# Performance work log

Hardware: AMD Instinct MI355X
Metric: run time of the kernel (lower is better)

The kernel has to match this reference:

```python
import jax, jax.numpy as jnp
import numpy as np

INPUT_SIZE = 24
OUTPUT_SIZE = 24
HIDDEN = 40
BATCH = 4096
SEQ = 256


def setup_inputs() -> dict:
    key = jax.random.key(0)
    ks = jax.random.split(key, 7)
    s = 1.0 / np.sqrt(HIDDEN)  # torch RNN/Linear default uniform bound
    x = jax.random.normal(ks[0], (BATCH, SEQ, INPUT_SIZE), dtype=jnp.float32)
    W_ih = jax.random.uniform(ks[1], (3 * HIDDEN, INPUT_SIZE), jnp.float32, -s, s)
    W_hh = jax.random.uniform(ks[2], (3 * HIDDEN, HIDDEN), jnp.float32, -s, s)
    b_ih = jax.random.uniform(ks[3], (3 * HIDDEN,), jnp.float32, -s, s)
    b_hh = jax.random.uniform(ks[4], (3 * HIDDEN,), jnp.float32, -s, s)
    W_fc = jax.random.uniform(ks[5], (OUTPUT_SIZE, HIDDEN), jnp.float32, -s, s)
    b_fc = jax.random.uniform(ks[6], (OUTPUT_SIZE,), jnp.float32, -s, s)
    return {"x": x, "W_ih": W_ih, "W_hh": W_hh, "b_ih": b_ih,
            "b_hh": b_hh, "W_fc": W_fc, "b_fc": b_fc}


def _gru_forward(x, W_ih, W_hh, b_ih, b_hh):
    # PyTorch GRU gate order: reset, update, new. Precompute input projections.
    B, T, _ = x.shape
    H = W_hh.shape[1]
    xg = jnp.einsum('bti,gi->btg', x, W_ih) + b_ih  # [B, T, 3H]

    def step(h, xg_t):
        hg = h @ W_hh.T + b_hh                      # [B, 3H]
        xr, xz, xn = jnp.split(xg_t, 3, axis=-1)
        hr, hz, hn = jnp.split(hg, 3, axis=-1)
        r = jax.nn.sigmoid(xr + hr)
        z = jax.nn.sigmoid(xz + hz)
        n = jnp.tanh(xn + r * hn)
        h_new = (1.0 - z) * n + z * h
        return h_new, h_new

    h0 = jnp.zeros((B, H), dtype=x.dtype)
    hT, outs = jax.lax.scan(step, h0, jnp.swapaxes(xg, 0, 1))  # outs: [T, B, H]
    return jnp.swapaxes(outs, 0, 1), hT                        # [B, T, H], [B, H]


def reference(x, W_ih, W_hh, b_ih, b_hh, W_fc, b_fc):
    seq_out, hT = _gru_forward(x, W_ih, W_hh, b_ih, b_hh)
    H = W_hh.shape[1]
    out = seq_out.reshape(-1, H)                   # [B*T, H]
    out = jax.nn.sigmoid(out @ W_fc.T + b_fc)      # [B*T, output_size]
    hidden = hT[None]                              # [n_layers=1, B, H]
    return out, hidden
```

## Files before the change

### kernel.cpp

```cpp
#include <hip/hip_runtime.h>
#include <math.h>

typedef __attribute__((ext_vector_type(8))) short short8;
typedef __attribute__((ext_vector_type(4))) float f32x4;

namespace {
constexpr int BATCH = 4096;
constexpr int SEQT  = 256;
constexpr int INSZ  = 24;
constexpr int H     = 40;
constexpr int NOUT  = 24;
constexpr int R     = 8;
constexpr int NT    = 256;

__device__ __forceinline__ unsigned short f2bf(float f) {
  unsigned int u = __float_as_uint(f);
  return (unsigned short)((u + 0x7FFFu + ((u >> 16) & 1u)) >> 16);
}
__device__ __forceinline__ unsigned short cvt_bf16(float f) {
  float r;
  asm("v_cvt_pk_bf16_f32 %0, %1, %2" : "=v"(r) : "v"(f), "v"(f));
  return (unsigned short)__float_as_uint(r);
}
__device__ __forceinline__ float4 ld4(const float* p) {
  return *reinterpret_cast<const float4*>(p);
}
__device__ __forceinline__ float sigm(float v) {
  return __builtin_amdgcn_rcpf(1.0f + __builtin_amdgcn_exp2f(v * -1.442695041f));
}
__device__ __forceinline__ float tanh_fast(float v) {
  return fmaf(2.0f,
              __builtin_amdgcn_rcpf(1.0f + __builtin_amdgcn_exp2f(v * -2.885390082f)),
              -1.0f);
}
}

#define BAR()                                              \
  asm volatile("s_waitcnt lgkmcnt(0)" ::: "memory");       \
  __builtin_amdgcn_s_barrier();                            \
  __builtin_amdgcn_sched_barrier(0);

__global__ __launch_bounds__(NT) void gru_mfma4(
    const float* __restrict__ x, const float* __restrict__ Wih,
    const float* __restrict__ Whh, const float* __restrict__ bih,
    const float* __restrict__ bhh, const float* __restrict__ Wfc,
    const float* __restrict__ bfc, float* __restrict__ out,
    float* __restrict__ hid) {
  __shared__ __align__(16) unsigned short Abuf[2 * 1024];

  const int tid = threadIdx.x;
  const int l   = tid & 63;
  const int w   = tid >> 6;
  const int lm  = l & 15;
  const int lq  = l >> 4;
  const int gb0 = blockIdx.x * R;

  reinterpret_cast<uint4*>(Abuf)[tid] = make_uint4(0, 0, 0, 0);

  const int aBase0 = ((lm * 64 + lq * 8)      ^ ((lm & 7) << 3));
  const int aBase1 = ((lm * 64 + lq * 8 + 32) ^ ((lm & 7) << 3));

  short8 B[4][2];
  float bias[4] = {0, 0, 0, 0};
  float hold[2] = {0, 0};
  int aw[2] = {0, 0};
  int u = 0;
  bool gvalid = false;
  if (w < 3) {
    u = w * 16 + lm;
    gvalid = (u < H);
#pragma unroll
    for (int z = 0; z < 4; ++z) {
#pragma unroll
      for (int kt = 0; kt < 2; ++kt) {
        short8 b;
#pragma unroll
        for (int j = 0; j < 8; ++j) {
          const int k = kt * 32 + lq * 8 + j;
          float v = 0.0f;
          if (gvalid) {
            if (z == 0)      v = (k < 24) ? Wih[u * 24 + k]          : Whh[u * 40 + (k - 24)];
            else if (z == 1) v = (k < 24) ? Wih[(40 + u) * 24 + k]   : Whh[(40 + u) * 40 + (k - 24)];
            else if (z == 2) v = (k < 24) ? Wih[(80 + u) * 24 + k]   : 0.0f;
            else             v = (k < 24) ? 0.0f                     : Whh[(80 + u) * 40 + (k - 24)];
          }
          b[j] = (short)f2bf(v);
        }
        B[z][kt] = b;
      }
    }
    if (gvalid) {
      bias[0] = bih[u] + bhh[u];
      bias[1] = bih[40 + u] + bhh[40 + u];
      bias[2] = bih[80 + u];
      bias[3] = bhh[80 + u];
    }
#pragma unroll
    for (int i = 0; i < 2; ++i) {
      const int arow = lq * 4 + i;
      aw[i] = ((arow * 64 + 24 + u) ^ ((arow & 7) << 3));
    }
  }

  short8 F[2][2];
  float biasF[2] = {0, 0};
  float* orow[2] = {nullptr, nullptr};
  const float* xp0 = nullptr;
  int xw0 = 0;
  bool xv = false;
  float4 xA0 = make_float4(0, 0, 0, 0), xB0 = make_float4(0, 0, 0, 0);
  if (w == 3) {
#pragma unroll
    for (int f = 0; f < 2; ++f) {
      const int o = f * 16 + lm;
#pragma unroll
      for (int kt = 0; kt < 2; ++kt) {
        short8 b;
#pragma unroll
        for (int j = 0; j < 8; ++j) {
          const int k = kt * 32 + lq * 8 + j;
          const float v = (o < NOUT && k >= 24) ? Wfc[o * H + (k - 24)] : 0.0f;
          b[j] = (short)f2bf(v);
        }
        F[f][kt] = b;
      }
      biasF[f] = (o < NOUT) ? bfc[o] : 0.0f;
    }
#pragma unroll
    for (int i = 0; i < 2; ++i)
      orow[i] = out + ((size_t)(gb0 + lq * 2 + i) * SEQT) * NOUT;

    xv = (l < 48);
    const int xr = l / 6, xc = (l - xr * 6) * 4;
    const int ar_ = ((xr >> 1) << 2) + (xr & 1);
    if (xv) xp0 = x + ((size_t)(gb0 + xr) * SEQT) * INSZ + xc;
    xw0 = ((ar_ * 64 + xc) ^ ((ar_ & 7) << 3));
  }

  __syncthreads();

  if (w == 3 && xv) {
    const float4 v0 = ld4(xp0);
    *reinterpret_cast<uint2*>(&Abuf[xw0]) = make_uint2(
        (unsigned)f2bf(v0.x) | ((unsigned)f2bf(v0.y) << 16),
        (unsigned)f2bf(v0.z) | ((unsigned)f2bf(v0.w) << 16));
    xA0 = ld4(xp0 + 1 * INSZ);
    xB0 = ld4(xp0 + 2 * INSZ);
  }
  __syncthreads();

#define GATE_STEP(BO, NBO)                                                      \
  if (w < 3) {                                                                  \
    const short8 A0 = *reinterpret_cast<const short8*>(&Abuf[(BO) + aBase0]);   \
    const short8 A1 = *reinterpret_cast<const short8*>(&Abuf[(BO) + aBase1]);   \
    f32x4 ar = {bias[0], bias[0], bias[0], bias[0]};                            \
    f32x4 az = {bias[1], bias[1], bias[1], bias[1]};                            \
    f32x4 ax = {bias[2], bias[2], bias[2], bias[2]};                            \
    f32x4 ah = {bias[3], bias[3], bias[3], bias[3]};                            \
    ar = __builtin_amdgcn_mfma_f32_16x16x32_bf16(A0, B[0][0], ar, 0, 0, 0);     \
    az = __builtin_amdgcn_mfma_f32_16x16x32_bf16(A0, B[1][0], az, 0, 0, 0);     \
    ax = __builtin_amdgcn_mfma_f32_16x16x32_bf16(A0, B[2][0], ax, 0, 0, 0);     \
    ah = __builtin_amdgcn_mfma_f32_16x16x32_bf16(A0, B[3][0], ah, 0, 0, 0);     \
    ar = __builtin_amdgcn_mfma_f32_16x16x32_bf16(A1, B[0][1], ar, 0, 0, 0);     \
    az = __builtin_amdgcn_mfma_f32_16x16x32_bf16(A1, B[1][1], az, 0, 0, 0);     \
    ah = __builtin_amdgcn_mfma_f32_16x16x32_bf16(A1, B[3][1], ah, 0, 0, 0);     \
    _Pragma("unroll")                                                           \
    for (int i = 0; i < 2; ++i) {                                               \
      const float rr = sigm(ar[i]);                                             \
      const float zz = sigm(az[i]);                                             \
      const float nn = tanh_fast(fmaf(rr, ah[i], ax[i]));                       \
      const float h  = fmaf(zz, hold[i] - nn, nn);                              \
      hold[i] = h;                                                              \
      if (gvalid) Abuf[(NBO) + aw[i]] = cvt_bf16(h);                            \
    }                                                                           \
  }

#define XSTAGE(T, TBO, XS)                                                      \
  if (xv) {                                                                     \
    if ((T) < SEQT) {                                                           \
      *reinterpret_cast<uint2*>(&Abuf[(TBO) + xw0]) = make_uint2(               \
          (unsigned)f2bf(XS.x) | ((unsigned)f2bf(XS.y) << 16),                  \
          (unsigned)f2bf(XS.z) | ((unsigned)f2bf(XS.w) << 16));                 \
    }                                                                           \
    if ((T) + 2 < SEQT) XS = ld4(xp0 + (size_t)((T) + 2) * INSZ);               \
  }

#define FC_STEP(T, BO)                                                          \
  {                                                                             \
    const short8 hA0 = *reinterpret_cast<const short8*>(&Abuf[(BO) + aBase0]);  \
    const short8 hA1 = *reinterpret_cast<const short8*>(&Abuf[(BO) + aBase1]);  \
    f32x4 f0 = {biasF[0], biasF[0], biasF[0], biasF[0]};                        \
    f32x4 f1 = {biasF[1], biasF[1], biasF[1], biasF[1]};                        \
    f0 = __builtin_amdgcn_mfma_f32_16x16x32_bf16(hA0, F[0][0], f0, 0, 0, 0);    \
    f1 = __builtin_amdgcn_mfma_f32_16x16x32_bf16(hA0, F[1][0], f1, 0, 0, 0);    \
    f0 = __builtin_amdgcn_mfma_f32_16x16x32_bf16(hA1, F[0][1], f0, 0, 0, 0);    \
    f1 = __builtin_amdgcn_mfma_f32_16x16x32_bf16(hA1, F[1][1], f1, 0, 0, 0);    \
    _Pragma("unroll")                                                           \
    for (int i = 0; i < 2; ++i) {                                               \
      orow[i][(size_t)(T) * NOUT + lm] = sigm(f0[i]);                           \
      if (lm < 8) orow[i][(size_t)(T) * NOUT + 16 + lm] = sigm(f1[i]);          \
    }                                                                           \
  }

  for (int tt = 0; tt < SEQT; tt += 2) {
    GATE_STEP(0, 1024)
    if (w == 3) {
      XSTAGE(tt + 1, 1024, xA0)
      if (tt > 0) FC_STEP(tt - 1, 0)
    }
    BAR()
    GATE_STEP(1024, 0)
    if (w == 3) {
      XSTAGE(tt + 2, 0, xB0)
      FC_STEP(tt, 1024)
    }
    BAR()
  }
  if (w == 3) FC_STEP(SEQT - 1, 0)

  if (w < 3 && gvalid) {
#pragma unroll
    for (int i = 0; i < 2; ++i)
      hid[(size_t)(gb0 + lq * 2 + i) * H + u] = hold[i];
  }
}

extern "C" void kernel_launch(void* const* d_in, const int* in_sizes, int n_in,
                              void* d_out, int out_size, void* d_ws, size_t ws_size,
                              hipStream_t stream) {
  const float* x   = (const float*)d_in[0];
  const float* Wih = (const float*)d_in[1];
  const float* Whh = (const float*)d_in[2];
  const float* bih = (const float*)d_in[3];
  const float* bhh = (const float*)d_in[4];
  const float* Wfc = (const float*)d_in[5];
  const float* bfc = (const float*)d_in[6];
  float* out = (float*)d_out;
  float* hid = out + (size_t)BATCH * SEQT * NOUT;

  dim3 grid(BATCH / R);
  dim3 block(NT);
  hipLaunchKernelGGL(gru_mfma4, grid, block, 0, stream,
                     x, Wih, Whh, bih, bhh, Wfc, bfc, out, hid);
}
```

Before: 122.4 us.

## Halve batch rows per block to double grid and shorten per-step gate work

Reduces the rows per block from 8 to 4, so the grid doubles to 1024 blocks. Each lane now processes a single MFMA output row (row 0 of each 4-row group), which halves the sigmoid/tanh and store work per step on the serial recurrence path. Packed bf16 conversion is also switched to the hardware cvt_pk instruction. In exchange, MFMA utilization drops (only 4 of 16 rows are useful), and there are more blocks to schedule. The x rounding mode also changes slightly.

Result: slower. 149.9 us (+22.4%).

```diff
diff --git a/kernel.cpp b/kernel.cpp
--- a/kernel.cpp
+++ b/kernel.cpp
@@ -10,7 +10,7 @@
 constexpr int INSZ  = 24;
 constexpr int H     = 40;
 constexpr int NOUT  = 24;
-constexpr int R     = 8;
+constexpr int R     = 4;
 constexpr int NT    = 256;
 
 __device__ __forceinline__ unsigned short f2bf(float f) {
@@ -21,6 +21,11 @@
   float r;
   asm("v_cvt_pk_bf16_f32 %0, %1, %2" : "=v"(r) : "v"(f), "v"(f));
   return (unsigned short)__float_as_uint(r);
+}
+__device__ __forceinline__ unsigned int cvt_pk2(float lo, float hi) {
+  float r;
+  asm("v_cvt_pk_bf16_f32 %0, %1, %2" : "=v"(r) : "v"(lo), "v"(hi));
+  return __float_as_uint(r);
 }
 __device__ __forceinline__ float4 ld4(const float* p) {
   return *reinterpret_cast<const float4*>(p);
@@ -62,8 +67,8 @@
 
   short8 B[4][2];
   float bias[4] = {0, 0, 0, 0};
-  float hold[2] = {0, 0};
-  int aw[2] = {0, 0};
+  float hold0 = 0.0f;
+  int aw0 = 0;
   int u = 0;
   bool gvalid = false;
   if (w < 3) {
@@ -95,16 +100,15 @@
       bias[2] = bih[80 + u];
       bias[3] = bhh[80 + u];
     }
-#pragma unroll
-    for (int i = 0; i < 2; ++i) {
-      const int arow = lq * 4 + i;
-      aw[i] = ((arow * 64 + 24 + u) ^ ((arow & 7) << 3));
+    {
+      const int arow = lq * 4;
+      aw0 = ((arow * 64 + 24 + u) ^ ((arow & 7) << 3));
     }
   }
 
   short8 F[2][2];
   float biasF[2] = {0, 0};
-  float* orow[2] = {nullptr, nullptr};
+  float* orow0 = nullptr;
   const float* xp0 = nullptr;
   int xw0 = 0;
   bool xv = false;
@@ -126,13 +130,11 @@
       }
       biasF[f] = (o < NOUT) ? bfc[o] : 0.0f;
     }
-#pragma unroll
-    for (int i = 0; i < 2; ++i)
-      orow[i] = out + ((size_t)(gb0 + lq * 2 + i) * SEQT) * NOUT;
-
-    xv = (l < 48);
+    orow0 = out + ((size_t)(gb0 + lq) * SEQT) * NOUT;
+
+    xv = (l < 24);
     const int xr = l / 6, xc = (l - xr * 6) * 4;
-    const int ar_ = ((xr >> 1) << 2) + (xr & 1);
+    const int ar_ = xr << 2;
     if (xv) xp0 = x + ((size_t)(gb0 + xr) * SEQT) * INSZ + xc;
     xw0 = ((ar_ * 64 + xc) ^ ((ar_ & 7) << 3));
   }
@@ -141,9 +143,8 @@
 
   if (w == 3 && xv) {
     const float4 v0 = ld4(xp0);
-    *reinterpret_cast<uint2*>(&Abuf[xw0]) = make_uint2(
-        (unsigned)f2bf(v0.x) | ((unsigned)f2bf(v0.y) << 16),
-        (unsigned)f2bf(v0.z) | ((unsigned)f2bf(v0.w) << 16));
+    *reinterpret_cast<uint2*>(&Abuf[xw0]) =
+        make_uint2(cvt_pk2(v0.x, v0.y), cvt_pk2(v0.z, v0.w));
     xA0 = ld4(xp0 + 1 * INSZ);
     xB0 = ld4(xp0 + 2 * INSZ);
   }
@@ -164,23 +165,21 @@
     ar = __builtin_amdgcn_mfma_f32_16x16x32_bf16(A1, B[0][1], ar, 0, 0, 0);     \
     az = __builtin_amdgcn_mfma_f32_16x16x32_bf16(A1, B[1][1], az, 0, 0, 0);     \
     ah = __builtin_amdgcn_mfma_f32_16x16x32_bf16(A1, B[3][1], ah, 0, 0, 0);     \
-    _Pragma("unroll")                                                           \
-    for (int i = 0; i < 2; ++i) {                                               \
-      const float rr = sigm(ar[i]);                                             \
-      const float zz = sigm(az[i]);                                             \
-      const float nn = tanh_fast(fmaf(rr, ah[i], ax[i]));                       \
-      const float h  = fmaf(zz, hold[i] - nn, nn);                              \
-      hold[i] = h;                                                              \
-      if (gvalid) Abuf[(NBO) + aw[i]] = cvt_bf16(h);                            \
+    {                                                                           \
+      const float rr = sigm(ar[0]);                                             \
+      const float zz = sigm(az[0]);                                             \
+      const float nn = tanh_fast(fmaf(rr, ah[0], ax[0]));                       \
+      const float h  = fmaf(zz, hold0 - nn, nn);                                \
+      hold0 = h;                                                                \
+      if (gvalid) Abuf[(NBO) + aw0] = cvt_bf16(h);                              \
     }                                                                           \
   }
 
 #define XSTAGE(T, TBO, XS)                                                      \
   if (xv) {                                                                     \
     if ((T) < SEQT) {                                                           \
-      *reinterpret_cast<uint2*>(&Abuf[(TBO) + xw0]) = make_uint2(               \
-          (unsigned)f2bf(XS.x) | ((unsigned)f2bf(XS.y) << 16),                  \
-          (unsigned)f2bf(XS.z) | ((unsigned)f2bf(XS.w) << 16));                 \
+      *reinterpret_cast<uint2*>(&Abuf[(TBO) + xw0]) =                           \
+          make_uint2(cvt_pk2(XS.x, XS.y), cvt_pk2(XS.z, XS.w));                 \
     }                                                                           \
     if ((T) + 2 < SEQT) XS = ld4(xp0 + (size_t)((T) + 2) * INSZ);               \
   }
@@ -195,11 +194,8 @@
     f1 = __builtin_amdgcn_mfma_f32_16x16x32_bf16(hA0, F[1][0], f1, 0, 0, 0);    \
     f0 = __builtin_amdgcn_mfma_f32_16x16x32_bf16(hA1, F[0][1], f0, 0, 0, 0);    \
     f1 = __builtin_amdgcn_mfma_f32_16x16x32_bf16(hA1, F[1][1], f1, 0, 0, 0);    \
-    _Pragma("unroll")                                                           \
-    for (int i = 0; i < 2; ++i) {                                               \
-      orow[i][(size_t)(T) * NOUT + lm] = sigm(f0[i]);                           \
-      if (lm < 8) orow[i][(size_t)(T) * NOUT + 16 + lm] = sigm(f1[i]);          \
-    }                                                                           \
+    orow0[(size_t)(T) * NOUT + lm] = sigm(f0[0]);                               \
+    if (lm < 8) orow0[(size_t)(T) * NOUT + 16 + lm] = sigm(f1[0]);              \
   }
 
   for (int tt = 0; tt < SEQT; tt += 2) {
@@ -218,11 +214,8 @@
   }
   if (w == 3) FC_STEP(SEQT - 1, 0)
 
-  if (w < 3 && gvalid) {
-#pragma unroll
-    for (int i = 0; i < 2; ++i)
-      hid[(size_t)(gb0 + lq * 2 + i) * H + u] = hold[i];
-  }
+  if (w < 3 && gvalid)
+    hid[(size_t)(gb0 + lq) * H + u] = hold0;
 }
 
 extern "C" void kernel_launch(void* const* d_in, const int* in_sizes, int n_in,
```

## Split GRU gate MFMA chains, raise gate-wave priority, deepen x prefetch

Applied to the files above, without the earlier changes.

Splits the dependent MFMA accumulation chain into two independent halves that are added afterwards, so the serial recurrence latency per step is shorter. Raises wave priority with s_setprio during the gate computation so it wins issue over the FC/staging wave. Deepens the x prefetch from 2 to 4 steps, unrolls the time loop by 4, and uses packed bf16 conversion instructions. Costs extra registers and a few extra adds per step.

Result: slower. 131.6 us (+7.5%).

```diff
diff --git a/kernel.cpp b/kernel.cpp
--- a/kernel.cpp
+++ b/kernel.cpp
@@ -21,6 +21,11 @@
   float r;
   asm("v_cvt_pk_bf16_f32 %0, %1, %2" : "=v"(r) : "v"(f), "v"(f));
   return (unsigned short)__float_as_uint(r);
+}
+__device__ __forceinline__ unsigned int cvt_pk2(float lo, float hi) {
+  float r;
+  asm("v_cvt_pk_bf16_f32 %0, %1, %2" : "=v"(r) : "v"(lo), "v"(hi));
+  return __float_as_uint(r);
 }
 __device__ __forceinline__ float4 ld4(const float* p) {
   return *reinterpret_cast<const float4*>(p);
@@ -108,7 +113,8 @@
   const float* xp0 = nullptr;
   int xw0 = 0;
   bool xv = false;
-  float4 xA0 = make_float4(0, 0, 0, 0), xB0 = make_float4(0, 0, 0, 0);
+  float4 xQ1 = make_float4(0,0,0,0), xQ2 = make_float4(0,0,0,0);
+  float4 xQ3 = make_float4(0,0,0,0), xQ0 = make_float4(0,0,0,0);
   if (w == 3) {
 #pragma unroll
     for (int f = 0; f < 2; ++f) {
@@ -141,48 +147,51 @@
 
   if (w == 3 && xv) {
     const float4 v0 = ld4(xp0);
-    *reinterpret_cast<uint2*>(&Abuf[xw0]) = make_uint2(
-        (unsigned)f2bf(v0.x) | ((unsigned)f2bf(v0.y) << 16),
-        (unsigned)f2bf(v0.z) | ((unsigned)f2bf(v0.w) << 16));
-    xA0 = ld4(xp0 + 1 * INSZ);
-    xB0 = ld4(xp0 + 2 * INSZ);
+    *reinterpret_cast<uint2*>(&Abuf[xw0]) =
+        make_uint2(cvt_pk2(v0.x, v0.y), cvt_pk2(v0.z, v0.w));
+    xQ1 = ld4(xp0 + 1 * INSZ);
+    xQ2 = ld4(xp0 + 2 * INSZ);
+    xQ3 = ld4(xp0 + 3 * INSZ);
+    xQ0 = ld4(xp0 + 4 * INSZ);
   }
   __syncthreads();
 
 #define GATE_STEP(BO, NBO)                                                      \
   if (w < 3) {                                                                  \
+    __builtin_amdgcn_s_setprio(1);                                              \
     const short8 A0 = *reinterpret_cast<const short8*>(&Abuf[(BO) + aBase0]);   \
     const short8 A1 = *reinterpret_cast<const short8*>(&Abuf[(BO) + aBase1]);   \
-    f32x4 ar = {bias[0], bias[0], bias[0], bias[0]};                            \
-    f32x4 az = {bias[1], bias[1], bias[1], bias[1]};                            \
-    f32x4 ax = {bias[2], bias[2], bias[2], bias[2]};                            \
-    f32x4 ah = {bias[3], bias[3], bias[3], bias[3]};                            \
-    ar = __builtin_amdgcn_mfma_f32_16x16x32_bf16(A0, B[0][0], ar, 0, 0, 0);     \
-    az = __builtin_amdgcn_mfma_f32_16x16x32_bf16(A0, B[1][0], az, 0, 0, 0);     \
-    ax = __builtin_amdgcn_mfma_f32_16x16x32_bf16(A0, B[2][0], ax, 0, 0, 0);     \
-    ah = __builtin_amdgcn_mfma_f32_16x16x32_bf16(A0, B[3][0], ah, 0, 0, 0);     \
-    ar = __builtin_amdgcn_mfma_f32_16x16x32_bf16(A1, B[0][1], ar, 0, 0, 0);     \
-    az = __builtin_amdgcn_mfma_f32_16x16x32_bf16(A1, B[1][1], az, 0, 0, 0);     \
-    ah = __builtin_amdgcn_mfma_f32_16x16x32_bf16(A1, B[3][1], ah, 0, 0, 0);     \
+    const f32x4 zed = {0.0f, 0.0f, 0.0f, 0.0f};                                 \
+    f32x4 ar0 = {bias[0], bias[0], bias[0], bias[0]};                           \
+    f32x4 az0 = {bias[1], bias[1], bias[1], bias[1]};                           \
+    f32x4 ax0 = {bias[2], bias[2], bias[2], bias[2]};                           \
+    f32x4 ah0 = {bias[3], bias[3], bias[3], bias[3]};                           \
+    ar0 = __builtin_amdgcn_mfma_f32_16x16x32_bf16(A0, B[0][0], ar0, 0, 0, 0);   \
+    az0 = __builtin_amdgcn_mfma_f32_16x16x32_bf16(A0, B[1][0], az0, 0, 0, 0);   \
+    ax0 = __builtin_amdgcn_mfma_f32_16x16x32_bf16(A0, B[2][0], ax0, 0, 0, 0);   \
+    ah0 = __builtin_amdgcn_mfma_f32_16x16x32_bf16(A0, B[3][0], ah0, 0, 0, 0);   \
+    f32x4 ar1 = __builtin_amdgcn_mfma_f32_16x16x32_bf16(A1, B[0][1], zed, 0, 0, 0); \
+    f32x4 az1 = __builtin_amdgcn_mfma_f32_16x16x32_bf16(A1, B[1][1], zed, 0, 0, 0); \
+    f32x4 ah1 = __builtin_amdgcn_mfma_f32_16x16x32_bf16(A1, B[3][1], zed, 0, 0, 0); \
     _Pragma("unroll")                                                           \
     for (int i = 0; i < 2; ++i) {                                               \
-      const float rr = sigm(ar[i]);                                             \
-      const float zz = sigm(az[i]);                                             \
-      const float nn = tanh_fast(fmaf(rr, ah[i], ax[i]));                       \
+      const float rr = sigm(ar0[i] + ar1[i]);                                   \
+      const float zz = sigm(az0[i] + az1[i]);                                   \
+      const float nn = tanh_fast(fmaf(rr, ah0[i] + ah1[i], ax0[i]));            \
       const float h  = fmaf(zz, hold[i] - nn, nn);                              \
       hold[i] = h;                                                              \
       if (gvalid) Abuf[(NBO) + aw[i]] = cvt_bf16(h);                            \
     }                                                                           \
+    __builtin_amdgcn_s_setprio(0);                                              \
   }
 
 #define XSTAGE(T, TBO, XS)                                                      \
   if (xv) {                                                                     \
     if ((T) < SEQT) {                                                           \
-      *reinterpret_cast<uint2*>(&Abuf[(TBO) + xw0]) = make_uint2(               \
-          (unsigned)f2bf(XS.x) | ((unsigned)f2bf(XS.y) << 16),                  \
-          (unsigned)f2bf(XS.z) | ((unsigned)f2bf(XS.w) << 16));                 \
+      *reinterpret_cast<uint2*>(&Abuf[(TBO) + xw0]) =                           \
+          make_uint2(cvt_pk2(XS.x, XS.y), cvt_pk2(XS.z, XS.w));                 \
     }                                                                           \
-    if ((T) + 2 < SEQT) XS = ld4(xp0 + (size_t)((T) + 2) * INSZ);               \
+    if ((T) + 4 < SEQT) XS = ld4(xp0 + (size_t)((T) + 4) * INSZ);               \
   }
 
 #define FC_STEP(T, BO)                                                          \
@@ -202,17 +211,29 @@
     }                                                                           \
   }
 
-  for (int tt = 0; tt < SEQT; tt += 2) {
+  for (int tt = 0; tt < SEQT; tt += 4) {
     GATE_STEP(0, 1024)
     if (w == 3) {
-      XSTAGE(tt + 1, 1024, xA0)
+      XSTAGE(tt + 1, 1024, xQ1)
       if (tt > 0) FC_STEP(tt - 1, 0)
     }
     BAR()
     GATE_STEP(1024, 0)
     if (w == 3) {
-      XSTAGE(tt + 2, 0, xB0)
+      XSTAGE(tt + 2, 0, xQ2)
       FC_STEP(tt, 1024)
+    }
+    BAR()
+    GATE_STEP(0, 1024)
+    if (w == 3) {
+      XSTAGE(tt + 3, 1024, xQ3)
+      FC_STEP(tt + 1, 0)
+    }
+    BAR()
+    GATE_STEP(1024, 0)
+    if (w == 3) {
+      XSTAGE(tt + 4, 0, xQ0)
+      FC_STEP(tt + 2, 1024)
     }
     BAR()
   }
```
